# Kernel tuning notes

Hardware: AMD Instinct MI355X
Metric: run time of the kernel (lower is better)

Reference implementation:

```python
import jax, jax.numpy as jnp
import numpy as np

B, S, D, H = 4, 1024, 512, 8
NEG = -1e9


def setup_inputs() -> dict:
    key = jax.random.key(0)
    ks = jax.random.split(key, 16)
    s = 0.02
    inp = {
        "query": jax.random.normal(ks[0], (B, S, D), dtype=jnp.float32),
        "key": jax.random.normal(ks[1], (B, S, D), dtype=jnp.float32),
        "value": jax.random.normal(ks[2], (B, S, D), dtype=jnp.float32),
        "mask": jax.random.randint(ks[3], (B, 1, S), 0, 2, dtype=jnp.int32),
        "mask_p": jax.random.randint(ks[4], (B, 1, S), 0, 2, dtype=jnp.int32),
        # multi-head projections: d_model -> d_model*h
        "Wq": jax.random.normal(ks[5], (D, H * D), dtype=jnp.float32) * s,
        "bq": jnp.zeros((H * D,), dtype=jnp.float32),
        "Wk": jax.random.normal(ks[6], (D, H * D), dtype=jnp.float32) * s,
        "bk": jnp.zeros((H * D,), dtype=jnp.float32),
        "Wv": jax.random.normal(ks[7], (D, H * D), dtype=jnp.float32) * s,
        "bv": jnp.zeros((H * D,), dtype=jnp.float32),
        # single-head p-branch projections: d_model -> d_model
        "Wpq": jax.random.normal(ks[8], (D, D), dtype=jnp.float32) * s,
        "bpq": jnp.zeros((D,), dtype=jnp.float32),
        "Wpk": jax.random.normal(ks[9], (D, D), dtype=jnp.float32) * s,
        "bpk": jnp.zeros((D,), dtype=jnp.float32),
        "Wpv": jax.random.normal(ks[10], (D, D), dtype=jnp.float32) * s,
        "bpv": jnp.zeros((D,), dtype=jnp.float32),
        # output projection
        "Wo": jax.random.normal(ks[11], (D, D), dtype=jnp.float32) * s,
        "bo": jnp.zeros((D,), dtype=jnp.float32),
    }
    return inp


def _attn(q, k, v, mask4):
    # q,k,v: [B,h,S,d]; mask4: [B,1,1,S] or None. Dropout omitted (eval mode).
    d = q.shape[-1]
    scores = jnp.einsum('bhqd,bhkd->bhqk', q, k) / jnp.sqrt(jnp.asarray(d, q.dtype))
    if mask4 is not None:
        scores = jnp.where(mask4 == 0, jnp.asarray(NEG, scores.dtype), scores)
    p = jax.nn.softmax(scores, axis=-1)
    return jnp.einsum('bhqk,bhkd->bhqd', p, v)


def reference(query, key, value, mask, mask_p,
              Wq, bq, Wk, bk, Wv, bv,
              Wpq, bpq, Wpk, bpk, Wpv, bpv, Wo, bo):
    nb, sl, d = query.shape
    def proj(x, W, b, heads):
        return (x @ W + b).reshape(nb, sl, heads, d).transpose(0, 2, 1, 3)

    m4 = mask[:, None, :, :]    # [B,1,1,S]
    mp4 = mask_p[:, None, :, :]

    qx = proj(query, Wq, bq, H)
    kx = proj(key, Wk, bk, H)
    vx = proj(value, Wv, bv, H)
    x = _attn(qx, kx, vx, m4)            # [B,H,S,D]

    qp = proj(query, Wpq, bpq, 1)
    kp = proj(key, Wpk, bpk, 1)
    vp = proj(value, Wpv, bpv, 1)
    x_p = _attn(qp, kp, vp, mp4)         # [B,1,S,D]

    # squared distance per head, softmax over heads at each (b, s)
    dis = jnp.sum((x - x_p) ** 2, axis=3)          # [B,H,S]
    w = jax.nn.softmax(1.0 / (dis + 1e-9), axis=1)  # [B,H,S]
    output = jnp.einsum('bhs,bhsd->bsd', w, x)      # [B,S,D]

    mixed = output * 0.8 + x_p[:, 0] * 0.2
    return mixed @ Wo + bo
```

## Files before the change

kernel.cpp:

```cpp
#include <hip/hip_runtime.h>
#include <cstdint>

#define S_LEN   1024
#define D_DIM   512
#define H_HEADS 8
#define B_BATCH 4
#define NEGV    -1000000000.0f

typedef __bf16 bf16;
typedef __bf16 bf16x8 __attribute__((ext_vector_type(8)));
typedef __bf16 bf16x4 __attribute__((ext_vector_type(4)));
typedef float  f32x4  __attribute__((ext_vector_type(4)));

#define GLL16(gp, lp) __builtin_amdgcn_global_load_lds( \
    (const __attribute__((address_space(1))) void*)(gp), \
    (__attribute__((address_space(3))) void*)(lp), 16, 0, 0)

#define VMW(N) asm volatile("s_waitcnt vmcnt(" #N ")" ::: "memory")
#define BARM() do { asm volatile("" ::: "memory"); \
                    __builtin_amdgcn_s_barrier();  \
                    asm volatile("" ::: "memory"); } while (0)

template<int MODE>
__global__ __launch_bounds__(512, 2) void gemm256_bt(
    const bf16* __restrict__ A, const bf16* __restrict__ B,
    void* __restrict__ Cout, const float* __restrict__ bias,
    const float* __restrict__ bias2, const int* __restrict__ mask,
    int N, int K, long zsA, long zsB, long zsC, float scale, int Hh)
{
  const int gx = gridDim.x, gy = gridDim.y;
  const int nwg = gx * gy * gridDim.z;
  int bid = blockIdx.x + gx * (blockIdx.y + gy * blockIdx.z);
  {
    const int q = nwg >> 3, r = nwg & 7;
    const int xcd = bid & 7, idx = bid >> 3;
    bid = (xcd < r ? xcd * (q + 1) : r * (q + 1) + (xcd - r) * q) + idx;
  }
  const int bx = bid % gx;
  const int by = (bid / gx) % gy;
  const int z  = bid / (gx * gy);

  A += (long)z * zsA;
  B += (long)z * zsB;
  const int bm0 = bx * 256;
  const int bn0 = by * 256;

  __shared__ __attribute__((aligned(16))) bf16 LDS[4 * 16384];

  const int tid  = threadIdx.x;
  const int wid  = tid >> 6;
  const int lane = tid & 63;
  const int wr = wid >> 2;
  const int wc = wid & 3;

  const long arow = (long)(bm0 + wid * 16 + (lane & 15)) * K + ((lane >> 4) * 8);
  const long brow = (long)(bn0 + wid * 16 + (lane & 15)) * K + ((lane >> 4) * 8);
  const long rstep = 128L * (long)K;

  auto stageA = [&](int tt) {
    bf16* d = LDS + (tt & 3) * 16384 + wid * 512;
    const bf16* g = A + arow + (long)tt * 32;
    GLL16(g, d);
    GLL16(g + rstep, d + 4096);
  };
  auto stageB = [&](int tt) {
    bf16* d = LDS + (tt & 3) * 16384 + 8192 + wid * 512;
    const bf16* g = B + brow + (long)tt * 32;
    GLL16(g, d);
    GLL16(g + rstep, d + 4096);
  };

  f32x4 acc[8][4] = {};
  const int NT = K >> 5;

  stageA(0); stageB(0);
  stageA(1); stageB(1);
  stageA(2); stageB(2);
  VMW(8);
  BARM();

  for (int t = 0; t < NT; ++t) {
    const bf16* bufp = LDS + (t & 3) * 16384;
    const bf16* ap = bufp + wr * 4096 + lane * 8;
    const bf16* bp = bufp + 8192 + wc * 2048 + lane * 8;

    if (t + 3 < NT) stageA(t + 3);
    bf16x8 a0[4], bb[4];
#pragma unroll
    for (int i = 0; i < 4; ++i) a0[i] = *(const bf16x8*)(ap + i * 512);
#pragma unroll
    for (int i = 0; i < 4; ++i) bb[i] = *(const bf16x8*)(bp + i * 512);
    BARM();
    __builtin_amdgcn_s_setprio(1);
#pragma unroll
    for (int mi = 0; mi < 4; ++mi)
#pragma unroll
      for (int ni = 0; ni < 4; ++ni)
        acc[mi][ni] = __builtin_amdgcn_mfma_f32_16x16x32_bf16(
            a0[mi], bb[ni], acc[mi][ni], 0, 0, 0);
    __builtin_amdgcn_s_setprio(0);
    BARM();

    if (t + 3 < NT) stageB(t + 3);
    bf16x8 a1[4];
#pragma unroll
    for (int i = 0; i < 4; ++i) a1[i] = *(const bf16x8*)(ap + (4 + i) * 512);
    BARM();
    __builtin_amdgcn_s_setprio(1);
#pragma unroll
    for (int mi = 0; mi < 4; ++mi)
#pragma unroll
      for (int ni = 0; ni < 4; ++ni)
        acc[4 + mi][ni] = __builtin_amdgcn_mfma_f32_16x16x32_bf16(
            a1[mi], bb[ni], acc[4 + mi][ni], 0, 0, 0);
    __builtin_amdgcn_s_setprio(0);
    if (t <= NT - 4)      VMW(8);
    else if (t == NT - 3) VMW(4);
    else if (t == NT - 2) VMW(0);
    BARM();
  }

  const int r0 = (lane >> 4) << 2;
  const int cn = lane & 15;

#pragma unroll
  for (int mi = 0; mi < 8; ++mi) {
#pragma unroll
    for (int ni = 0; ni < 4; ++ni) {
      const int n = bn0 + wc * 64 + ni * 16 + cn;
      float bv = 0.f;
      if constexpr (MODE != 4) {
        const float* bp2 = (z == 1 && bias2) ? bias2 : bias;
        if (bp2) bv = bp2[n];
      }
      int mk = 1;
      if constexpr (MODE == 4) mk = mask[(z / Hh) * S_LEN + n];
#pragma unroll
      for (int r = 0; r < 4; ++r) {
        const int m = bm0 + wr * 128 + mi * 16 + r0 + r;
        float v = acc[mi][ni][r];
        if constexpr (MODE == 1) {
          long o = (long)z * zsC +
                   (((long)(m >> 10) * Hh + (n >> 9)) * S_LEN + (m & (S_LEN - 1))) * D_DIM
                   + (n & (D_DIM - 1));
          ((bf16*)Cout)[o] = (bf16)(v + bv);
        } else if constexpr (MODE == 2) {
          long o = (long)z * zsC +
                   (((long)(m >> 10) * Hh + (n >> 9)) * D_DIM + (n & (D_DIM - 1))) * S_LEN
                   + (m & (S_LEN - 1));
          ((bf16*)Cout)[o] = (bf16)(v + bv);
        } else if constexpr (MODE == 3) {
          ((float*)Cout)[(long)z * zsC + (long)m * N + n] = v + bv;
        } else {
          float sv = (mk == 0) ? NEGV : v * scale;
          ((bf16*)Cout)[(long)z * zsC + (long)m * N + n] = (bf16)sv;
        }
      }
    }
  }
}

template<int MODE>
__global__ __launch_bounds__(256) void gemm_bt(
    const bf16* __restrict__ A, const bf16* __restrict__ B,
    void* __restrict__ Cout, const float* __restrict__ bias,
    const float* __restrict__ bias2, const int* __restrict__ mask,
    int N, int K, long zsA, long zsB, long zsC, float scale, int Hh)
{
  const int z = blockIdx.z;
  A += (long)z * zsA;
  B += (long)z * zsB;

  const int bm0 = blockIdx.x * 128;
  const int bn0 = blockIdx.y * 128;

  __shared__ __attribute__((aligned(16))) bf16 As[128 * 32];
  __shared__ __attribute__((aligned(16))) bf16 Bs[128 * 32];

  const int tid  = threadIdx.x;
  const int wid  = tid >> 6;
  const int lane = tid & 63;
  const int wm = (wid >> 1) * 64;
  const int wn = (wid & 1) * 64;

  const int srow = tid >> 2;
  const int scol = (tid & 3) * 8;
  const bf16* gA0 = A + (long)(bm0 + srow) * K + scol;
  const bf16* gA1 = A + (long)(bm0 + 64 + srow) * K + scol;
  const bf16* gB0 = B + (long)(bn0 + srow) * K + scol;
  const bf16* gB1 = B + (long)(bn0 + 64 + srow) * K + scol;
  bf16* lA0 = As + tid * 8;
  bf16* lA1 = As + 2048 + tid * 8;
  bf16* lB0 = Bs + tid * 8;
  bf16* lB1 = Bs + 2048 + tid * 8;

  const int lrow = lane & 15;
  const int lk   = (lane >> 4) * 8;
  const bf16* fA = As + (wm + lrow) * 32 + lk;
  const bf16* fB = Bs + (wn + lrow) * 32 + lk;

  f32x4 acc[4][4] = {};

  for (int k0 = 0; k0 < K; k0 += 32) {
    GLL16(gA0 + k0, lA0);
    GLL16(gA1 + k0, lA1);
    GLL16(gB0 + k0, lB0);
    GLL16(gB1 + k0, lB1);
    __syncthreads();
    bf16x8 af[4], bfr[4];
#pragma unroll
    for (int i = 0; i < 4; ++i) af[i]  = *(const bf16x8*)(fA + i * 16 * 32);
#pragma unroll
    for (int i = 0; i < 4; ++i) bfr[i] = *(const bf16x8*)(fB + i * 16 * 32);
#pragma unroll
    for (int mi = 0; mi < 4; ++mi)
#pragma unroll
      for (int ni = 0; ni < 4; ++ni)
        acc[mi][ni] = __builtin_amdgcn_mfma_f32_16x16x32_bf16(
            af[mi], bfr[ni], acc[mi][ni], 0, 0, 0);
    __syncthreads();
  }

  const int r0 = (lane >> 4) << 2;
  const int cn = lane & 15;

#pragma unroll
  for (int mi = 0; mi < 4; ++mi) {
#pragma unroll
    for (int ni = 0; ni < 4; ++ni) {
      const int n = bn0 + wn + ni * 16 + cn;
      float bv = 0.f;
      if constexpr (MODE != 4) {
        const float* bp = (z == 1 && bias2) ? bias2 : bias;
        if (bp) bv = bp[n];
      }
      int mk = 1;
      if constexpr (MODE == 4) mk = mask[(z / Hh) * S_LEN + n];
#pragma unroll
      for (int r = 0; r < 4; ++r) {
        const int m = bm0 + wm + mi * 16 + r0 + r;
        float v = acc[mi][ni][r];
        if constexpr (MODE == 0) {
          ((bf16*)Cout)[(long)z * zsC + (long)m * N + n] = (bf16)(v + bv);
        } else if constexpr (MODE == 2) {
          long o = (long)z * zsC +
                   (((long)(m >> 10) * Hh + (n >> 9)) * D_DIM + (n & (D_DIM - 1))) * S_LEN
                   + (m & (S_LEN - 1));
          ((bf16*)Cout)[o] = (bf16)(v + bv);
        } else if constexpr (MODE == 3) {
          ((float*)Cout)[(long)z * zsC + (long)m * N + n] = v + bv;
        } else if constexpr (MODE == 4) {
          float sv = (mk == 0) ? NEGV : v * scale;
          ((bf16*)Cout)[(long)z * zsC + (long)m * N + n] = (bf16)sv;
        }
      }
    }
  }
}

__global__ __launch_bounds__(256) void softmax_rows(bf16* __restrict__ buf)
{
  const long row = blockIdx.x;
  bf16* p = buf + row * S_LEN;
  const int tid = threadIdx.x;
  const int wid = tid >> 6, lane = tid & 63;
  bf16x4 raw = *(const bf16x4*)(p + tid * 4);
  float v[4];
#pragma unroll
  for (int j = 0; j < 4; ++j) v[j] = (float)raw[j];
  float mx = fmaxf(fmaxf(v[0], v[1]), fmaxf(v[2], v[3]));
  for (int m = 32; m; m >>= 1) mx = fmaxf(mx, __shfl_xor(mx, m, 64));
  __shared__ float red[4];
  if (lane == 0) red[wid] = mx;
  __syncthreads();
  mx = fmaxf(fmaxf(red[0], red[1]), fmaxf(red[2], red[3]));
  float e[4]; float s = 0.f;
#pragma unroll
  for (int j = 0; j < 4; ++j) { e[j] = __expf(v[j] - mx); s += e[j]; }
  for (int m = 32; m; m >>= 1) s += __shfl_xor(s, m, 64);
  __syncthreads();
  if (lane == 0) red[wid] = s;
  __syncthreads();
  s = red[0] + red[1] + red[2] + red[3];
  const float inv = 1.f / s;
  bf16x4 o;
#pragma unroll
  for (int j = 0; j < 4; ++j) o[j] = (bf16)(e[j] * inv);
  *(bf16x4*)(p + tid * 4) = o;
}

__global__ __launch_bounds__(256) void combine_kernel(
    const float* __restrict__ X, const float* __restrict__ XP,
    bf16* __restrict__ MIX)
{
  const int m = blockIdx.x;
  const int b = m >> 10;
  const int s = m & (S_LEN - 1);
  const int tid = threadIdx.x;
  const int wid = tid >> 6, lane = tid & 63;
  const float2 xp = *(const float2*)(XP + (long)m * D_DIM + tid * 2);
  float xv0[H_HEADS], xv1[H_HEADS], part[H_HEADS];
#pragma unroll
  for (int h = 0; h < H_HEADS; ++h) {
    const float* xrow = X + ((long)(b * H_HEADS + h) * S_LEN + s) * D_DIM;
    float2 t = *(const float2*)(xrow + tid * 2);
    xv0[h] = t.x; xv1[h] = t.y;
    float d0 = t.x - xp.x, d1 = t.y - xp.y;
    part[h] = d0 * d0 + d1 * d1;
  }
  __shared__ float red[4][H_HEADS];
#pragma unroll
  for (int h = 0; h < H_HEADS; ++h) {
    float v = part[h];
    for (int mm = 32; mm; mm >>= 1) v += __shfl_xor(v, mm, 64);
    if (lane == 0) red[wid][h] = v;
  }
  __syncthreads();
  float w[H_HEADS]; float mx = -1e30f;
#pragma unroll
  for (int h = 0; h < H_HEADS; ++h) {
    float dis = red[0][h] + red[1][h] + red[2][h] + red[3][h];
    w[h] = 1.f / (dis + 1e-9f);
    mx = fmaxf(mx, w[h]);
  }
  float ssum = 0.f;
#pragma unroll
  for (int h = 0; h < H_HEADS; ++h) { w[h] = __expf(w[h] - mx); ssum += w[h]; }
  const float inv = 1.f / ssum;
  float m0 = 0.f, m1 = 0.f;
#pragma unroll
  for (int h = 0; h < H_HEADS; ++h) { m0 += w[h] * xv0[h]; m1 += w[h] * xv1[h]; }
  m0 = 0.8f * m0 * inv + 0.2f * xp.x;
  m1 = 0.8f * m1 * inv + 0.2f * xp.y;
  const bf16 h0 = (bf16)m0, h1 = (bf16)m1;
  const bf16 l0 = (bf16)(m0 - (float)h0), l1 = (bf16)(m1 - (float)h1);
  bf16* orow = MIX + (long)m * 1536;
  orow[tid * 2]        = h0; orow[tid * 2 + 1]        = h1;
  orow[512 + tid * 2]  = l0; orow[512 + tid * 2 + 1]  = l1;
  orow[1024 + tid * 2] = h0; orow[1024 + tid * 2 + 1] = h1;
}

__global__ __launch_bounds__(256) void cvt3_kernel(
    const float* __restrict__ s0, const float* __restrict__ s1, const float* __restrict__ s2,
    bf16* __restrict__ d0, bf16* __restrict__ d1, bf16* __restrict__ d2)
{
  const float* s = blockIdx.z == 0 ? s0 : (blockIdx.z == 1 ? s1 : s2);
  bf16* d       = blockIdx.z == 0 ? d0 : (blockIdx.z == 1 ? d1 : d2);
  const long i = ((long)blockIdx.x * 256 + threadIdx.x) * 8;
  float4 a = *(const float4*)(s + i);
  float4 b = *(const float4*)(s + i + 4);
  bf16x8 o;
  o[0]=(bf16)a.x; o[1]=(bf16)a.y; o[2]=(bf16)a.z; o[3]=(bf16)a.w;
  o[4]=(bf16)b.x; o[5]=(bf16)b.y; o[6]=(bf16)b.z; o[7]=(bf16)b.w;
  *(bf16x8*)(d + i) = o;
}

template<int TRIPLE>
__global__ __launch_bounds__(256) void transpose_cvt3(
    const float* __restrict__ s0, const float* __restrict__ s1, const float* __restrict__ s2,
    bf16* __restrict__ d0, bf16* __restrict__ d1, bf16* __restrict__ d2,
    int R, int C)
{
  const float* src = blockIdx.z == 0 ? s0 : (blockIdx.z == 1 ? s1 : s2);
  bf16* dst       = blockIdx.z == 0 ? d0 : (blockIdx.z == 1 ? d1 : d2);
  __shared__ float t[32][33];
  const int tc = threadIdx.x & 31;
  const int tr = threadIdx.x >> 5;
  const int c0 = blockIdx.x * 32, r0 = blockIdx.y * 32;
#pragma unroll
  for (int i = 0; i < 4; ++i)
    t[tr + 8 * i][tc] = src[(long)(r0 + tr + 8 * i) * C + c0 + tc];
  __syncthreads();
  const int RD = TRIPLE ? 3 * R : R;
#pragma unroll
  for (int i = 0; i < 4; ++i) {
    float v = t[tc][tr + 8 * i];
    long o = (long)(c0 + tr + 8 * i) * RD + r0 + tc;
    const bf16 hi = (bf16)v;
    dst[o] = hi;
    if (TRIPLE) {
      dst[o + R] = hi;
      dst[o + 2 * R] = (bf16)(v - (float)hi);
    }
  }
}

extern "C" void kernel_launch(void* const* d_in, const int* in_sizes, int n_in,
                              void* d_out, int out_size, void* d_ws, size_t ws_size,
                              hipStream_t stream) {
  const float* query  = (const float*)d_in[0];
  const float* key    = (const float*)d_in[1];
  const float* value  = (const float*)d_in[2];
  const int*   mask   = (const int*)d_in[3];
  const int*   mask_p = (const int*)d_in[4];
  const float* Wq  = (const float*)d_in[5];  const float* bq  = (const float*)d_in[6];
  const float* Wk  = (const float*)d_in[7];  const float* bk  = (const float*)d_in[8];
  const float* Wv  = (const float*)d_in[9];  const float* bv  = (const float*)d_in[10];
  const float* Wpq = (const float*)d_in[11]; const float* bpq = (const float*)d_in[12];
  const float* Wpk = (const float*)d_in[13]; const float* bpk = (const float*)d_in[14];
  const float* Wpv = (const float*)d_in[15]; const float* bpv = (const float*)d_in[16];
  const float* Wo  = (const float*)d_in[17]; const float* bo  = (const float*)d_in[18];

  char* ws = (char*)d_ws;
  size_t off = 0;
  auto alloc = [&](size_t bytes) -> void* {
    void* p = ws + off;
    off += (bytes + 255) & ~(size_t)255;
    return p;
  };
  const long BS  = (long)B_BATCH * S_LEN;
  const long ZSD = (long)S_LEN * D_DIM;
  const long ZSS = (long)S_LEN * S_LEN;
  const long SD  = BS * D_DIM;

  bf16* WQT  = (bf16*)alloc(SD * 2);
  bf16* WKT  = (bf16*)alloc(SD * 2);
  bf16* WVT  = (bf16*)alloc(SD * 2);
  bf16* WPQT = (bf16*)alloc((long)D_DIM * D_DIM * 2);
  bf16* WPKT = (bf16*)alloc((long)D_DIM * D_DIM * 2);
  bf16* WPVT = (bf16*)alloc((long)D_DIM * D_DIM * 2);
  bf16* WOT3 = (bf16*)alloc((long)D_DIM * 3 * D_DIM * 2);
  bf16* XQ16 = (bf16*)alloc(SD * 2);
  bf16* XK16 = (bf16*)alloc(SD * 2);
  bf16* XV16 = (bf16*)alloc(SD * 2);
  bf16* MIX  = XQ16;
  bf16* Q16  = (bf16*)alloc((long)H_HEADS * SD * 2);
  bf16* K16  = (bf16*)alloc((long)H_HEADS * SD * 2);
  float* X   = (float*)Q16;
  bf16* VT16 = (bf16*)alloc((long)H_HEADS * SD * 2);
  bf16* QP16 = (bf16*)alloc(SD * 2);
  bf16* KP16 = (bf16*)alloc(SD * 2);
  float* XP  = (float*)QP16;
  bf16* VPT16= (bf16*)alloc(SD * 2);
  bf16* SC   = (bf16*)alloc((long)B_BATCH * H_HEADS * ZSS * 2);
  bf16* SCP  = (bf16*)alloc((long)B_BATCH * ZSS * 2);
  (void)in_sizes; (void)n_in; (void)out_size; (void)SCP;

  if (off > ws_size) return;

  const dim3 blk(256);
  const dim3 blk512(512);
  const float scale = 0.044194173824159216f;

  cvt3_kernel<<<dim3(1024, 1, 3), blk, 0, stream>>>(query, key, value, XQ16, XK16, XV16);
  transpose_cvt3<0><<<dim3(128, 16, 3), blk, 0, stream>>>(Wq, Wk, Wv, WQT, WKT, WVT, 512, 4096);
  transpose_cvt3<0><<<dim3(16, 16, 3), blk, 0, stream>>>(Wpq, Wpk, Wpv, WPQT, WPKT, WPVT, 512, 512);
  transpose_cvt3<1><<<dim3(16, 16, 1), blk, 0, stream>>>(Wo, Wo, Wo, WOT3, WOT3, WOT3, 512, 512);

  gemm256_bt<1><<<dim3(16, 16, 2), blk512, 0, stream>>>(XQ16, WQT, Q16, bq, bk, nullptr,
      4096, 512, SD, SD, (long)H_HEADS * SD, 1.f, H_HEADS);
  gemm256_bt<2><<<dim3(16, 16, 1), blk512, 0, stream>>>(XV16, WVT, VT16, bv, nullptr, nullptr,
      4096, 512, 0, 0, 0, 1.f, H_HEADS);
  gemm_bt<0><<<dim3(32, 4, 2), blk, 0, stream>>>(XQ16, WPQT, QP16, bpq, bpk, nullptr,
      512, 512, SD, (long)D_DIM * D_DIM, SD, 1.f, 1);
  gemm_bt<2><<<dim3(32, 4, 1), blk, 0, stream>>>(XV16, WPVT, VPT16, bpv, nullptr, nullptr,
      512, 512, 0, 0, 0, 1.f, 1);

  gemm256_bt<4><<<dim3(4, 4, 32), blk512, 0, stream>>>(Q16, K16, SC, nullptr, nullptr, mask,
      1024, 512, ZSD, ZSD, ZSS, scale, H_HEADS);
  gemm_bt<4><<<dim3(8, 8, 4), blk, 0, stream>>>(QP16, KP16, SCP, nullptr, nullptr, mask_p,
      1024, 512, ZSD, ZSD, ZSS, scale, 1);

  softmax_rows<<<dim3(32768 + 4096), blk, 0, stream>>>(SC);

  gemm256_bt<3><<<dim3(4, 2, 32), blk512, 0, stream>>>(SC, VT16, X, nullptr, nullptr, nullptr,
      512, 1024, ZSS, ZSD, ZSD, 1.f, 1);
  gemm_bt<3><<<dim3(8, 4, 4), blk, 0, stream>>>(SCP, VPT16, XP, nullptr, nullptr, nullptr,
      512, 1024, ZSS, ZSD, ZSD, 1.f, 1);

  combine_kernel<<<dim3(4096), blk, 0, stream>>>(X, XP, MIX);

  gemm_bt<3><<<dim3(32, 4, 1), blk, 0, stream>>>(MIX, WOT3, d_out, bo, nullptr, nullptr,
      512, 1536, 0, 0, 0, 1.f, 1);
}
```

Measured before the change: 477.7 us.

## Fold single-head p-branch into multi-head GEMMs as a ninth head

```diff
diff --git a/kernel.cpp b/kernel.cpp
--- a/kernel.cpp
+++ b/kernel.cpp
@@ -26,7 +26,8 @@
     const bf16* __restrict__ A, const bf16* __restrict__ B,
     void* __restrict__ Cout, const float* __restrict__ bias,
     const float* __restrict__ bias2, const int* __restrict__ mask,
-    int N, int K, long zsA, long zsB, long zsC, float scale, int Hh)
+    const int* __restrict__ maskp,
+    int N, int K, long zsA, long zsB, long zsC, float scale)
 {
   const int gx = gridDim.x, gy = gridDim.y;
   const int nwg = gx * gy * gridDim.z;
@@ -84,13 +85,16 @@
     const bf16* ap = bufp + wr * 4096 + lane * 8;
     const bf16* bp = bufp + 8192 + wc * 2048 + lane * 8;
 
-    if (t + 3 < NT) stageA(t + 3);
-    bf16x8 a0[4], bb[4];
+    if (t + 3 < NT) { stageA(t + 3); stageB(t + 3); }
+
+    bf16x8 a0[4], a1[4], bb[4];
 #pragma unroll
     for (int i = 0; i < 4; ++i) a0[i] = *(const bf16x8*)(ap + i * 512);
 #pragma unroll
     for (int i = 0; i < 4; ++i) bb[i] = *(const bf16x8*)(bp + i * 512);
-    BARM();
+#pragma unroll
+    for (int i = 0; i < 4; ++i) a1[i] = *(const bf16x8*)(ap + (4 + i) * 512);
+
     __builtin_amdgcn_s_setprio(1);
 #pragma unroll
     for (int mi = 0; mi < 4; ++mi)
@@ -98,15 +102,6 @@
       for (int ni = 0; ni < 4; ++ni)
         acc[mi][ni] = __builtin_amdgcn_mfma_f32_16x16x32_bf16(
             a0[mi], bb[ni], acc[mi][ni], 0, 0, 0);
-    __builtin_amdgcn_s_setprio(0);
-    BARM();
-
-    if (t + 3 < NT) stageB(t + 3);
-    bf16x8 a1[4];
-#pragma unroll
-    for (int i = 0; i < 4; ++i) a1[i] = *(const bf16x8*)(ap + (4 + i) * 512);
-    BARM();
-    __builtin_amdgcn_s_setprio(1);
 #pragma unroll
     for (int mi = 0; mi < 4; ++mi)
 #pragma unroll
@@ -114,6 +109,7 @@
         acc[4 + mi][ni] = __builtin_amdgcn_mfma_f32_16x16x32_bf16(
             a1[mi], bb[ni], acc[4 + mi][ni], 0, 0, 0);
     __builtin_amdgcn_s_setprio(0);
+
     if (t <= NT - 4)      VMW(8);
     else if (t == NT - 3) VMW(4);
     else if (t == NT - 2) VMW(0);
@@ -134,19 +130,22 @@
         if (bp2) bv = bp2[n];
       }
       int mk = 1;
-      if constexpr (MODE == 4) mk = mask[(z / Hh) * S_LEN + n];
+      if constexpr (MODE == 4) {
+        const int* mp = (z >= 32 ? maskp : mask);
+        mk = mp[(z & 3) * S_LEN + n];
+      }
 #pragma unroll
       for (int r = 0; r < 4; ++r) {
         const int m = bm0 + wr * 128 + mi * 16 + r0 + r;
         float v = acc[mi][ni][r];
         if constexpr (MODE == 1) {
           long o = (long)z * zsC +
-                   (((long)(m >> 10) * Hh + (n >> 9)) * S_LEN + (m & (S_LEN - 1))) * D_DIM
+                   (((long)(n >> 9) * B_BATCH + (m >> 10)) * S_LEN + (m & (S_LEN - 1))) * D_DIM
                    + (n & (D_DIM - 1));
           ((bf16*)Cout)[o] = (bf16)(v + bv);
         } else if constexpr (MODE == 2) {
           long o = (long)z * zsC +
-                   (((long)(m >> 10) * Hh + (n >> 9)) * D_DIM + (n & (D_DIM - 1))) * S_LEN
+                   (((long)(n >> 9) * B_BATCH + (m >> 10)) * D_DIM + (n & (D_DIM - 1))) * S_LEN
                    + (m & (S_LEN - 1));
           ((bf16*)Cout)[o] = (bf16)(v + bv);
         } else if constexpr (MODE == 3) {
@@ -230,32 +229,19 @@
     for (int ni = 0; ni < 4; ++ni) {
       const int n = bn0 + wn + ni * 16 + cn;
       float bv = 0.f;
-      if constexpr (MODE != 4) {
-        const float* bp = (z == 1 && bias2) ? bias2 : bias;
-        if (bp) bv = bp[n];
-      }
-      int mk = 1;
-      if constexpr (MODE == 4) mk = mask[(z / Hh) * S_LEN + n];
+      const float* bp = (z == 1 && bias2) ? bias2 : bias;
+      if (bp) bv = bp[n];
 #pragma unroll
       for (int r = 0; r < 4; ++r) {
         const int m = bm0 + wm + mi * 16 + r0 + r;
         float v = acc[mi][ni][r];
-        if constexpr (MODE == 0) {
-          ((bf16*)Cout)[(long)z * zsC + (long)m * N + n] = (bf16)(v + bv);
-        } else if constexpr (MODE == 2) {
-          long o = (long)z * zsC +
-                   (((long)(m >> 10) * Hh + (n >> 9)) * D_DIM + (n & (D_DIM - 1))) * S_LEN
-                   + (m & (S_LEN - 1));
-          ((bf16*)Cout)[o] = (bf16)(v + bv);
-        } else if constexpr (MODE == 3) {
+        if constexpr (MODE == 3) {
           ((float*)Cout)[(long)z * zsC + (long)m * N + n] = v + bv;
-        } else if constexpr (MODE == 4) {
-          float sv = (mk == 0) ? NEGV : v * scale;
-          ((bf16*)Cout)[(long)z * zsC + (long)m * N + n] = (bf16)sv;
         }
       }
     }
   }
+  (void)mask; (void)scale; (void)Hh;
 }
 
 __global__ __launch_bounds__(256) void softmax_rows(bf16* __restrict__ buf)
@@ -302,7 +288,7 @@
   float xv0[H_HEADS], xv1[H_HEADS], part[H_HEADS];
 #pragma unroll
   for (int h = 0; h < H_HEADS; ++h) {
-    const float* xrow = X + ((long)(b * H_HEADS + h) * S_LEN + s) * D_DIM;
+    const float* xrow = X + ((long)(h * B_BATCH + b) * S_LEN + s) * D_DIM;
     float2 t = *(const float2*)(xrow + tid * 2);
     xv0[h] = t.x; xv1[h] = t.y;
     float d0 = t.x - xp.x, d1 = t.y - xp.y;
@@ -353,6 +339,20 @@
   o[0]=(bf16)a.x; o[1]=(bf16)a.y; o[2]=(bf16)a.z; o[3]=(bf16)a.w;
   o[4]=(bf16)b.x; o[5]=(bf16)b.y; o[6]=(bf16)b.z; o[7]=(bf16)b.w;
   *(bf16x8*)(d + i) = o;
+}
+
+__global__ __launch_bounds__(256) void concat_bias(
+    const float* __restrict__ b0, const float* __restrict__ p0,
+    const float* __restrict__ b1, const float* __restrict__ p1,
+    const float* __restrict__ b2, const float* __restrict__ p2,
+    float* __restrict__ o0, float* __restrict__ o1, float* __restrict__ o2)
+{
+  const int i = blockIdx.x * 256 + threadIdx.x;
+  const float* bb; const float* pp; float* oo;
+  if (blockIdx.y == 0)      { bb = b0; pp = p0; oo = o0; }
+  else if (blockIdx.y == 1) { bb = b1; pp = p1; oo = o1; }
+  else                      { bb = b2; pp = p2; oo = o2; }
+  oo[i] = (i < 4096) ? bb[i] : pp[i - 4096];
 }
 
 template<int TRIPLE>
@@ -408,33 +408,35 @@
     off += (bytes + 255) & ~(size_t)255;
     return p;
   };
-  const long BS  = (long)B_BATCH * S_LEN;
-  const long ZSD = (long)S_LEN * D_DIM;
-  const long ZSS = (long)S_LEN * S_LEN;
-  const long SD  = BS * D_DIM;
+  const long BS   = (long)B_BATCH * S_LEN;
+  const long ZSD  = (long)S_LEN * D_DIM;
+  const long ZSS  = (long)S_LEN * S_LEN;
+  const long SD   = BS * D_DIM;
+  const long DD   = (long)D_DIM * D_DIM;
+  const long WSTR = SD + DD;
+  const long HSD  = 9L * B_BATCH * ZSD;
 
   bf16* WQT  = (bf16*)alloc(SD * 2);
+  bf16* WPQT = (bf16*)alloc(DD * 2);
   bf16* WKT  = (bf16*)alloc(SD * 2);
+  bf16* WPKT = (bf16*)alloc(DD * 2);
   bf16* WVT  = (bf16*)alloc(SD * 2);
-  bf16* WPQT = (bf16*)alloc((long)D_DIM * D_DIM * 2);
-  bf16* WPKT = (bf16*)alloc((long)D_DIM * D_DIM * 2);
-  bf16* WPVT = (bf16*)alloc((long)D_DIM * D_DIM * 2);
-  bf16* WOT3 = (bf16*)alloc((long)D_DIM * 3 * D_DIM * 2);
+  bf16* WPVT = (bf16*)alloc(DD * 2);
+  bf16* WOT3 = (bf16*)alloc(3 * DD * 2);
+  float* BQ9 = (float*)alloc(4608 * 4);
+  float* BK9 = (float*)alloc(4608 * 4);
+  float* BV9 = (float*)alloc(4608 * 4);
   bf16* XQ16 = (bf16*)alloc(SD * 2);
   bf16* XK16 = (bf16*)alloc(SD * 2);
   bf16* XV16 = (bf16*)alloc(SD * 2);
   bf16* MIX  = XQ16;
-  bf16* Q16  = (bf16*)alloc((long)H_HEADS * SD * 2);
-  bf16* K16  = (bf16*)alloc((long)H_HEADS * SD * 2);
+  bf16* Q16  = (bf16*)alloc(HSD * 2);
+  bf16* K16  = (bf16*)alloc(HSD * 2);
   float* X   = (float*)Q16;
-  bf16* VT16 = (bf16*)alloc((long)H_HEADS * SD * 2);
-  bf16* QP16 = (bf16*)alloc(SD * 2);
-  bf16* KP16 = (bf16*)alloc(SD * 2);
-  float* XP  = (float*)QP16;
-  bf16* VPT16= (bf16*)alloc(SD * 2);
-  bf16* SC   = (bf16*)alloc((long)B_BATCH * H_HEADS * ZSS * 2);
-  bf16* SCP  = (bf16*)alloc((long)B_BATCH * ZSS * 2);
-  (void)in_sizes; (void)n_in; (void)out_size; (void)SCP;
+  float* XP  = X + 32 * ZSD;
+  bf16* VT9  = (bf16*)alloc(HSD * 2);
+  bf16* SC   = (bf16*)alloc(36L * ZSS * 2);
+  (void)in_sizes; (void)n_in; (void)out_size;
 
   if (off > ws_size) return;
 
@@ -443,30 +445,23 @@
   const float scale = 0.044194173824159216f;
 
   cvt3_kernel<<<dim3(1024, 1, 3), blk, 0, stream>>>(query, key, value, XQ16, XK16, XV16);
+  concat_bias<<<dim3(18, 3), blk, 0, stream>>>(bq, bpq, bk, bpk, bv, bpv, BQ9, BK9, BV9);
   transpose_cvt3<0><<<dim3(128, 16, 3), blk, 0, stream>>>(Wq, Wk, Wv, WQT, WKT, WVT, 512, 4096);
   transpose_cvt3<0><<<dim3(16, 16, 3), blk, 0, stream>>>(Wpq, Wpk, Wpv, WPQT, WPKT, WPVT, 512, 512);
   transpose_cvt3<1><<<dim3(16, 16, 1), blk, 0, stream>>>(Wo, Wo, Wo, WOT3, WOT3, WOT3, 512, 512);
 
-  gemm256_bt<1><<<dim3(16, 16, 2), blk512, 0, stream>>>(XQ16, WQT, Q16, bq, bk, nullptr,
-      4096, 512, SD, SD, (long)H_HEADS * SD, 1.f, H_HEADS);
-  gemm256_bt<2><<<dim3(16, 16, 1), blk512, 0, stream>>>(XV16, WVT, VT16, bv, nullptr, nullptr,
-      4096, 512, 0, 0, 0, 1.f, H_HEADS);
-  gemm_bt<0><<<dim3(32, 4, 2), blk, 0, stream>>>(XQ16, WPQT, QP16, bpq, bpk, nullptr,
-      512, 512, SD, (long)D_DIM * D_DIM, SD, 1.f, 1);
-  gemm_bt<2><<<dim3(32, 4, 1), blk, 0, stream>>>(XV16, WPVT, VPT16, bpv, nullptr, nullptr,
-      512, 512, 0, 0, 0, 1.f, 1);
-
-  gemm256_bt<4><<<dim3(4, 4, 32), blk512, 0, stream>>>(Q16, K16, SC, nullptr, nullptr, mask,
-      1024, 512, ZSD, ZSD, ZSS, scale, H_HEADS);
-  gemm_bt<4><<<dim3(8, 8, 4), blk, 0, stream>>>(QP16, KP16, SCP, nullptr, nullptr, mask_p,
-      1024, 512, ZSD, ZSD, ZSS, scale, 1);
-
-  softmax_rows<<<dim3(32768 + 4096), blk, 0, stream>>>(SC);
-
-  gemm256_bt<3><<<dim3(4, 2, 32), blk512, 0, stream>>>(SC, VT16, X, nullptr, nullptr, nullptr,
-      512, 1024, ZSS, ZSD, ZSD, 1.f, 1);
-  gemm_bt<3><<<dim3(8, 4, 4), blk, 0, stream>>>(SCP, VPT16, XP, nullptr, nullptr, nullptr,
-      512, 1024, ZSS, ZSD, ZSD, 1.f, 1);
+  gemm256_bt<1><<<dim3(16, 18, 2), blk512, 0, stream>>>(XQ16, WQT, Q16, BQ9, BK9,
+      nullptr, nullptr, 4608, 512, SD, WSTR, HSD, 1.f);
+  gemm256_bt<2><<<dim3(16, 18, 1), blk512, 0, stream>>>(XV16, WVT, VT9, BV9, nullptr,
+      nullptr, nullptr, 4608, 512, 0, 0, 0, 1.f);
+
+  gemm256_bt<4><<<dim3(4, 4, 36), blk512, 0, stream>>>(Q16, K16, SC, nullptr, nullptr,
+      mask, mask_p, 1024, 512, ZSD, ZSD, ZSS, scale);
+
+  softmax_rows<<<dim3(36864), blk, 0, stream>>>(SC);
+
+  gemm256_bt<3><<<dim3(4, 2, 36), blk512, 0, stream>>>(SC, VT9, X, nullptr, nullptr,
+      nullptr, nullptr, 512, 1024, ZSS, ZSD, ZSD, 1.f);
 
   combine_kernel<<<dim3(4096), blk, 0, stream>>>(X, XP, MIX);
 
```

New measurement: 495.5 us. 3.7% more time.
